# Optimization experiments

Measured on AMD Instinct MI355X. Metric: run time of the kernel, lower is better.

Reference implementation:

```python
import jax, jax.numpy as jnp
import numpy as np

B = 32; LS = 512; LABEL = 256; PRED = 256; LD = 512   # LD = LS//2 + PRED
CIN = 21; COUT = 21; D = 512; H = 8; E = 64; M = 64   # M = top frequency modes
DFF = 2048; LE = 2; MARK = 4; K = 25; EPS = 1e-5


def moving_mean(x):
    # series_decomp moving average: edge-replicate pad then window mean (via cumsum)
    p = (K - 1) // 2
    xp = jnp.pad(x, ((0, 0), (p, p), (0, 0)), mode='edge')
    c = jnp.cumsum(xp, axis=1)
    c = jnp.concatenate([jnp.zeros_like(c[:, :1]), c], axis=1)
    return (c[:, K:] - c[:, :-K]) / K


def decomp(x):
    m = moving_mean(x)
    return x - m, m   # (high/seasonal, low/trend)


def circ_conv(x, k):  # x [B,L,C], k [3,C,O], kernel-3 circular conv, no bias
    xp = jnp.pad(x, ((0, 0), (1, 1), (0, 0)), mode='wrap')
    return jax.lax.conv_general_dilated(xp, k, (1,), 'VALID', dimension_numbers=('NWC', 'WIO', 'NWC'))


def embed(x, mark, ck, tw):  # DataEmbedding_wo_pos: token conv + timeF linear
    return circ_conv(x, ck) + mark @ tw


def heads(x):  # [B,L,D] -> [B,L,H,E]
    return x.reshape(x.shape[0], x.shape[1], H, E)


def freq_self(q, wre, wim):  # FrequencyAdaptiveAttention; q [B,L,H,E]
    L = q.shape[1]
    x = jnp.transpose(q, (0, 2, 3, 1))            # [B,H,E,L]
    xf = jnp.fft.rfft(x, axis=-1)                 # [B,H,E,Lf]
    amp = jnp.mean(jnp.abs(xf), axis=(0, 1, 2))   # adaptive mode selection
    _, idx = jax.lax.top_k(amp, M)
    xs = xf[..., idx]                             # [B,H,E,M]
    w = (wre + 1j * wim).astype(xs.dtype)         # [H,E,E,M] complex
    outs = jnp.einsum('bhem,heom->bhom', xs, w)
    oft = jnp.zeros(xf.shape, xf.dtype).at[..., idx].set(outs)
    y = jnp.fft.irfft(oft, n=L, axis=-1)
    return jnp.transpose(y, (0, 3, 1, 2))         # [B,L,H,E]


def freq_cross(q, k, wre, wim):  # AlignmentFrequencyAttention
    Lq = q.shape[1]
    qf = jnp.fft.rfft(jnp.transpose(q, (0, 2, 3, 1)), axis=-1)
    kf = jnp.fft.rfft(jnp.transpose(k, (0, 2, 3, 1)), axis=-1)
    _, qi = jax.lax.top_k(jnp.mean(jnp.abs(qf), axis=(0, 1, 2)), M)
    _, ki = jax.lax.top_k(jnp.mean(jnp.abs(kf), axis=(0, 1, 2)), M)
    qs = qf[..., qi]; ks = kf[..., ki]            # [B,H,E,M]
    qk = jnp.tanh(jnp.einsum('bhex,bhey->bhxy', qs, ks))
    qkv = jnp.einsum('bhxy,bhey->bhex', qk, ks)
    w = (wre + 1j * wim).astype(qs.dtype)
    outs = jnp.einsum('bhex,heox->bhox', qkv, w)
    oft = jnp.zeros(qf.shape, qf.dtype).at[..., qi].set(outs)
    y = jnp.fft.irfft(oft / (D * D), n=Lq, axis=-1)
    return jnp.transpose(y, (0, 3, 1, 2))


def my_layernorm(x, g, b):  # LN then subtract time-mean (Autoformer my_Layernorm)
    mu = jnp.mean(x, -1, keepdims=True)
    var = jnp.var(x, -1, keepdims=True)
    xh = (x - mu) * jax.lax.rsqrt(var + EPS) * g + b
    return xh - jnp.mean(xh, axis=1, keepdims=True)


def _forward(x_enc, x_mark_enc, x_dec, x_mark_dec, emb_enc_k, emb_enc_t, emb_dec_k, emb_dec_t, fw_enc_re, fw_enc_im, fw_dec_re, fw_dec_im, fw_cr_re, fw_cr_im, enc_Wq, enc_bq, enc_Wo, enc_bo, enc_c1, enc_c2, enc_ng, enc_nb, ds_Wq, ds_bq, ds_Wo, ds_bo, dc_Wq, dc_bq, dc_Wk, dc_bk, dc_Wo, dc_bo, dec_c1, dec_c2, dec_tp, dec_ng, dec_nb, proj_W, proj_b):
    mean = jnp.broadcast_to(jnp.mean(x_enc, axis=1, keepdims=True), (B, PRED, CIN))
    high_init, low_init = decomp(x_enc)
    low_init = jnp.concatenate([low_init[:, -LABEL:, :], mean], axis=1)       # [B,LD,CIN]
    high_init = jnp.pad(high_init[:, -LABEL:, :], ((0, 0), (0, PRED), (0, 0)))
    # encoder
    enc = embed(x_enc, x_mark_enc, emb_enc_k, emb_enc_t)                      # [B,LS,D]
    for i in range(LE):
        a = freq_self(heads(enc @ enc_Wq[i] + enc_bq[i]), fw_enc_re, fw_enc_im)
        a = a.reshape(B, LS, D) @ enc_Wo[i] + enc_bo[i]
        x1, _ = decomp(enc + a)
        y = jax.nn.gelu(x1 @ enc_c1[i]) @ enc_c2[i]
        enc, _ = decomp(x1 + y)
    enc = my_layernorm(enc, enc_ng, enc_nb)
    # decoder (1 layer)
    dec = embed(high_init, x_mark_dec, emb_dec_k, emb_dec_t)                  # [B,LD,D]
    a = freq_self(heads(dec @ ds_Wq + ds_bq), fw_dec_re, fw_dec_im)
    a = a.reshape(B, LD, D) @ ds_Wo + ds_bo
    x1, t1 = decomp(dec + a)
    c = freq_cross(heads(x1 @ dc_Wq + dc_bq), heads(enc @ dc_Wk + dc_bk), fw_cr_re, fw_cr_im)
    c = c.reshape(B, LD, D) @ dc_Wo + dc_bo
    x2, t2 = decomp(x1 + c)
    y = jax.nn.gelu(x2 @ dec_c1) @ dec_c2
    x3, t3 = decomp(x2 + y)
    low_part = low_init + circ_conv(t1 + t2 + t3, dec_tp)                     # trend branch
    high_part = my_layernorm(x3, dec_ng, dec_nb) @ proj_W + proj_b            # seasonal branch
    return (low_part + high_part)[:, -PRED:, :]


def setup_inputs():
    key = jax.random.key(0)
    ks = jax.random.split(key, 32)
    r = lambda i, shape, s=1.0: jax.random.normal(ks[i], shape, dtype=jnp.float32) * s
    z = lambda shape: jnp.zeros(shape, jnp.float32)
    sd = D ** -0.5
    return {
        'x_enc': r(0, (B, LS, CIN)), 'x_mark_enc': r(1, (B, LS, MARK)),
        'x_dec': r(2, (B, LD, CIN)), 'x_mark_dec': r(3, (B, LD, MARK)),
        'emb_enc_k': r(4, (3, CIN, D), 0.1), 'emb_enc_t': r(5, (MARK, D), 0.1),
        'emb_dec_k': r(6, (3, CIN, D), 0.1), 'emb_dec_t': r(7, (MARK, D), 0.1),
        'fw_enc_re': r(8, (H, E, E, M), 0.02), 'fw_enc_im': r(9, (H, E, E, M), 0.02),
        'fw_dec_re': r(10, (H, E, E, M), 0.02), 'fw_dec_im': r(11, (H, E, E, M), 0.02),
        'fw_cr_re': r(12, (H, E, E, M), 0.02), 'fw_cr_im': r(13, (H, E, E, M), 0.02),
        'enc_Wq': r(14, (LE, D, D), sd), 'enc_bq': z((LE, D)),
        'enc_Wo': r(15, (LE, D, D), sd), 'enc_bo': z((LE, D)),
        'enc_c1': r(16, (LE, D, DFF), sd), 'enc_c2': r(17, (LE, DFF, D), DFF ** -0.5),
        'enc_ng': jnp.ones((D,), jnp.float32), 'enc_nb': z((D,)),
        'ds_Wq': r(18, (D, D), sd), 'ds_bq': z((D,)),
        'ds_Wo': r(19, (D, D), sd), 'ds_bo': z((D,)),
        'dc_Wq': r(20, (D, D), sd), 'dc_bq': z((D,)),
        'dc_Wk': r(21, (D, D), sd), 'dc_bk': z((D,)),
        'dc_Wo': r(22, (D, D), sd), 'dc_bo': z((D,)),
        'dec_c1': r(23, (D, DFF), sd), 'dec_c2': r(24, (DFF, D), DFF ** -0.5),
        'dec_tp': r(25, (3, D, COUT), sd),
        'dec_ng': jnp.ones((D,), jnp.float32), 'dec_nb': z((D,)),
        'proj_W': r(26, (D, COUT), sd), 'proj_b': z((COUT,)),
    }


def reference(x_enc, x_mark_enc, x_dec, x_mark_dec, emb_enc_k, emb_enc_t, emb_dec_k, emb_dec_t, fw_enc_re, fw_enc_im, fw_dec_re, fw_dec_im, fw_cr_re, fw_cr_im, enc_Wq, enc_bq, enc_Wo, enc_bo, enc_c1, enc_c2, enc_ng, enc_nb, ds_Wq, ds_bq, ds_Wo, ds_bo, dc_Wq, dc_bq, dc_Wk, dc_bk, dc_Wo, dc_bo, dec_c1, dec_c2, dec_tp, dec_ng, dec_nb, proj_W, proj_b):
    return _forward(x_enc, x_mark_enc, x_dec, x_mark_dec, emb_enc_k, emb_enc_t, emb_dec_k, emb_dec_t, fw_enc_re, fw_enc_im, fw_dec_re, fw_dec_im, fw_cr_re, fw_cr_im, enc_Wq, enc_bq, enc_Wo, enc_bo, enc_c1, enc_c2, enc_ng, enc_nb, ds_Wq, ds_bq, ds_Wo, ds_bo, dc_Wq, dc_bq, dc_Wk, dc_bk, dc_Wo, dc_bo, dec_c1, dec_c2, dec_tp, dec_ng, dec_nb, proj_W, proj_b)
```

## Files before the change

kernel.cpp:

```cpp
#include <hip/hip_runtime.h>
#include <math.h>

#define B_    32
#define LQ    512
#define CIN_  21
#define COUT_ 21
#define D_    512
#define H_    8
#define E_    64
#define M_    64
#define DFF_  2048
#define MARK_ 4
#define KWIN  25
#define PW    12
#define LF    257
#define PRED_ 256
#define EPS_  1e-5f

static __device__ __forceinline__ int iclamp(int v, int lo, int hi) {
  return v < lo ? lo : (v > hi ? hi : v);
}

__global__ void k_dft_tables(float* __restrict__ cosF, float* __restrict__ negsinF,
                             float* __restrict__ c512, float* __restrict__ s512) {
  int i = blockIdx.x * 256 + threadIdx.x;
  if (i < 512) {
    float th = (float)i * (6.283185307179586f / 512.0f);
    c512[i] = cosf(th);
    s512[i] = sinf(th);
  }
  if (i >= 512 * LF) return;
  int t = i / LF, f = i % LF;
  int r = (t * f) & 511;
  float th = (float)r * (6.283185307179586f / 512.0f);
  cosF[i] = cosf(th);
  negsinF[i] = -sinf(th);
}

__global__ void k_enc_decomp(const float* __restrict__ x,
                             float* __restrict__ lowi, float* __restrict__ highi) {
  int b = blockIdx.x, c = threadIdx.x;
  if (c >= CIN_) return;
  const float* xb = x + (long)b * LQ * CIN_ + c;
  float s = 0.f;
  for (int t = 0; t < LQ; t++) s += xb[(long)t * CIN_];
  float mean = s / (float)LQ;
  for (int t = 256; t < LQ; t++) {
    float w = 0.f;
    for (int j = t - PW; j <= t + PW; j++) {
      int jj = iclamp(j, 0, LQ - 1);
      w += xb[(long)jj * CIN_];
    }
    float m = w * (1.f / KWIN);
    lowi [((long)b * LQ + (t - 256)) * CIN_ + c] = m;
    highi[((long)b * LQ + (t - 256)) * CIN_ + c] = xb[(long)t * CIN_] - m;
  }
  for (int t = 256; t < LQ; t++) {
    lowi [((long)b * LQ + t) * CIN_ + c] = mean;
    highi[((long)b * LQ + t) * CIN_ + c] = 0.f;
  }
}

__global__ void k_embed(const float* __restrict__ x, const float* __restrict__ mark,
                        const float* __restrict__ ck, const float* __restrict__ tw,
                        float* __restrict__ out) {
  int o = blockIdx.x * 256 + threadIdx.x;
  int t = blockIdx.y, b = blockIdx.z;
  float acc = 0.f;
  const float* xb = x + (long)b * LQ * CIN_;
  #pragma unroll
  for (int j = 0; j < 3; j++) {
    int tt = (t + j - 1 + LQ) & (LQ - 1);
    const float* xr = xb + (long)tt * CIN_;
    const float* kr = ck + (long)(j * CIN_) * D_ + o;
    for (int c = 0; c < CIN_; c++) acc = fmaf(xr[c], kr[(long)c * D_], acc);
  }
  const float* mr = mark + ((long)b * LQ + t) * MARK_;
  #pragma unroll
  for (int mm = 0; mm < MARK_; mm++) acc = fmaf(mr[mm], tw[(long)mm * D_ + o], acc);
  out[((long)b * LQ + t) * D_ + o] = acc;
}

template<int ACT>
__global__ __launch_bounds__(256) void k_gemm(
    const float* __restrict__ A, const float* __restrict__ Bm,
    const float* __restrict__ bias, float* __restrict__ C,
    int Mr, int Nd, int Kd) {
  constexpr int BM = 128, BN = 128, BK = 32, SA = BM + 1;
  __shared__ float As[BK][SA];
  __shared__ float Bs[BK][BN];
  int m0 = blockIdx.y * BM, n0 = blockIdx.x * BN;
  int tid = threadIdx.x;
  int tx = tid & 15, ty = tid >> 4;
  float acc[8][8] = {};
  const float* Ag = A + (long)m0 * Kd;
  for (int k0 = 0; k0 < Kd; k0 += BK) {
    #pragma unroll
    for (int r = 0; r < 4; r++) {
      int slot = tid + r * 256;
      int row = slot >> 3, k4 = slot & 7;
      const float4 v = *(const float4*)&Ag[(long)row * Kd + k0 + k4 * 4];
      As[k4 * 4 + 0][row] = v.x; As[k4 * 4 + 1][row] = v.y;
      As[k4 * 4 + 2][row] = v.z; As[k4 * 4 + 3][row] = v.w;
    }
    #pragma unroll
    for (int r = 0; r < 4; r++) {
      int slot = tid + r * 256;
      int kk = slot >> 5, n4 = slot & 31;
      *(float4*)&Bs[kk][n4 * 4] = *(const float4*)&Bm[(long)(k0 + kk) * Nd + n0 + n4 * 4];
    }
    __syncthreads();
    #pragma unroll
    for (int kk = 0; kk < BK; kk++) {
      float av[8], bv[8];
      #pragma unroll
      for (int i = 0; i < 8; i++) av[i] = As[kk][ty * 8 + i];
      #pragma unroll
      for (int j = 0; j < 8; j++) bv[j] = Bs[kk][tx * 8 + j];
      #pragma unroll
      for (int i = 0; i < 8; i++)
        #pragma unroll
        for (int j = 0; j < 8; j++)
          acc[i][j] = fmaf(av[i], bv[j], acc[i][j]);
    }
    __syncthreads();
  }
  float bj[8];
  #pragma unroll
  for (int j = 0; j < 8; j++) bj[j] = bias ? bias[n0 + tx * 8 + j] : 0.f;
  #pragma unroll
  for (int i = 0; i < 8; i++) {
    long gm = m0 + ty * 8 + i;
    float* Crow = C + gm * Nd + n0 + tx * 8;
    #pragma unroll
    for (int j4 = 0; j4 < 2; j4++) {
      float4 v;
      float t0[4];
      #pragma unroll
      for (int j = 0; j < 4; j++) {
        float x = acc[i][j4 * 4 + j] + bj[j4 * 4 + j];
        if (ACT == 1) {
          float x3 = x * x * x;
          float th = tanhf(0.7978845608028654f * (x + 0.044715f * x3));
          x = 0.5f * x * (1.f + th);
        }
        t0[j] = x;
      }
      v.x = t0[0]; v.y = t0[1]; v.z = t0[2]; v.w = t0[3];
      *(float4*)&Crow[j4 * 4] = v;
    }
  }
}

__global__ void k_zero(float* __restrict__ p, int n) {
  int i = blockIdx.x * 256 + threadIdx.x;
  if (i < n) p[i] = 0.f;
}

__global__ __launch_bounds__(256) void k_specamp(
    const float* __restrict__ X, const float* __restrict__ cosT,
    const float* __restrict__ nsinT, float* __restrict__ amp) {
  int m0 = blockIdx.y * 64, n0 = blockIdx.x * 64;
  int tid = threadIdx.x, tx = tid & 15, ty = tid >> 4;
  __shared__ float As[32][64];
  __shared__ float Cs[32][65];
  __shared__ float Ss[32][65];
  float aR[4][4] = {}, aI[4][4] = {};
  int b = m0 >> 9, d0 = m0 & 511;
  const float* Xb = X + (long)b * LQ * D_ + d0;
  for (int k0 = 0; k0 < 512; k0 += 32) {
    {
      int mm = tid & 63, kk0 = tid >> 6;
      #pragma unroll
      for (int r = 0; r < 8; r++) {
        int kk = kk0 + r * 4;
        As[kk][mm] = Xb[(long)(k0 + kk) * D_ + mm];
      }
    }
    {
      int nn = tid & 63, kk0 = tid >> 6;
      #pragma unroll
      for (int r = 0; r < 8; r++) {
        int kk = kk0 + r * 4;
        int gn = n0 + nn;
        float c = 0.f, s = 0.f;
        if (gn < LF) { long a = (long)(k0 + kk) * LF + gn; c = cosT[a]; s = nsinT[a]; }
        Cs[kk][nn] = c; Ss[kk][nn] = s;
      }
    }
    __syncthreads();
    #pragma unroll
    for (int kk = 0; kk < 32; kk++) {
      float av[4], cv[4], sv[4];
      #pragma unroll
      for (int i = 0; i < 4; i++) av[i] = As[kk][ty * 4 + i];
      #pragma unroll
      for (int j = 0; j < 4; j++) { cv[j] = Cs[kk][tx * 4 + j]; sv[j] = Ss[kk][tx * 4 + j]; }
      #pragma unroll
      for (int i = 0; i < 4; i++)
        #pragma unroll
        for (int j = 0; j < 4; j++) {
          aR[i][j] = fmaf(av[i], cv[j], aR[i][j]);
          aI[i][j] = fmaf(av[i], sv[j], aI[i][j]);
        }
    }
    __syncthreads();
  }
  __shared__ float csum[64];
  if (tid < 64) csum[tid] = 0.f;
  __syncthreads();
  #pragma unroll
  for (int j = 0; j < 4; j++) {
    float s = 0.f;
    #pragma unroll
    for (int i = 0; i < 4; i++) s += sqrtf(aR[i][j] * aR[i][j] + aI[i][j] * aI[i][j]);
    atomicAdd(&csum[tx * 4 + j], s);
  }
  __syncthreads();
  if (tid < 64 && n0 + tid < LF) atomicAdd(&amp[n0 + tid], csum[tid]);
}

__global__ void k_topk(const float* __restrict__ amp, int* __restrict__ idx) {
  __shared__ float v[512];
  __shared__ float rv[512];
  __shared__ int   ri[512];
  int tid = threadIdx.x;
  v[tid] = (tid < LF) ? amp[tid] : -INFINITY;
  __syncthreads();
  for (int k = 0; k < M_; k++) {
    rv[tid] = v[tid]; ri[tid] = tid;
    __syncthreads();
    for (int st = 256; st > 0; st >>= 1) {
      if (tid < st) {
        float a = rv[tid], b = rv[tid + st];
        int ai = ri[tid], bi = ri[tid + st];
        if (b > a || (b == a && bi < ai)) { rv[tid] = b; ri[tid] = bi; }
      }
      __syncthreads();
    }
    if (tid == 0) { idx[k] = ri[0]; v[ri[0]] = -INFINITY; }
    __syncthreads();
  }
}

__global__ __launch_bounds__(256) void k_gatherdft(
    const float* __restrict__ X, const float* __restrict__ cosT,
    const float* __restrict__ nsinT, const int* __restrict__ idx,
    float* __restrict__ gR, float* __restrict__ gI) {
  int m0 = blockIdx.x * 64;
  int tid = threadIdx.x, tx = tid & 15, ty = tid >> 4;
  __shared__ float As[32][64];
  __shared__ float Cs[32][65];
  __shared__ float Ss[32][65];
  __shared__ int fsel[64];
  if (tid < 64) fsel[tid] = idx[tid];
  __syncthreads();
  float aR[4][4] = {}, aI[4][4] = {};
  int b = m0 >> 9, d0 = m0 & 511;
  const float* Xb = X + (long)b * LQ * D_ + d0;
  for (int k0 = 0; k0 < 512; k0 += 32) {
    {
      int mm = tid & 63, kk0 = tid >> 6;
      #pragma unroll
      for (int r = 0; r < 8; r++) {
        int kk = kk0 + r * 4;
        As[kk][mm] = Xb[(long)(k0 + kk) * D_ + mm];
      }
    }
    {
      int nn = tid & 63, kk0 = tid >> 6;
      int f = fsel[nn];
      #pragma unroll
      for (int r = 0; r < 8; r++) {
        int kk = kk0 + r * 4;
        long a = (long)(k0 + kk) * LF + f;
        Cs[kk][nn] = cosT[a]; Ss[kk][nn] = nsinT[a];
      }
    }
    __syncthreads();
    #pragma unroll
    for (int kk = 0; kk < 32; kk++) {
      float av[4], cv[4], sv[4];
      #pragma unroll
      for (int i = 0; i < 4; i++) av[i] = As[kk][ty * 4 + i];
      #pragma unroll
      for (int j = 0; j < 4; j++) { cv[j] = Cs[kk][tx * 4 + j]; sv[j] = Ss[kk][tx * 4 + j]; }
      #pragma unroll
      for (int i = 0; i < 4; i++)
        #pragma unroll
        for (int j = 0; j < 4; j++) {
          aR[i][j] = fmaf(av[i], cv[j], aR[i][j]);
          aI[i][j] = fmaf(av[i], sv[j], aI[i][j]);
        }
    }
    __syncthreads();
  }
  #pragma unroll
  for (int i = 0; i < 4; i++) {
    long row = m0 + ty * 4 + i;
    #pragma unroll
    for (int j = 0; j < 4; j++) {
      gR[row * 64 + tx * 4 + j] = aR[i][j];
      gI[row * 64 + tx * 4 + j] = aI[i][j];
    }
  }
}

__global__ __launch_bounds__(256) void k_modemix(
    const float* __restrict__ sre, const float* __restrict__ sim,
    const float* __restrict__ wre, const float* __restrict__ wim,
    float* __restrict__ ore, float* __restrict__ oim) {
  int b = blockIdx.z, h = blockIdx.y, oc = blockIdx.x;
  int m = threadIdx.x, osub = threadIdx.y;
  int o = oc * 4 + osub;
  __shared__ float xr[E_][M_], xi[E_][M_];
  #pragma unroll
  for (int r = 0; r < 16; r++) {
    int e = r * 4 + osub;
    long a = ((long)(b * H_ + h) * E_ + e) * M_ + m;
    xr[e][m] = sre[a]; xi[e][m] = sim[a];
  }
  __syncthreads();
  float ar = 0.f, ai = 0.f;
  const float* wrb = wre + ((long)(h * E_) * E_ + o) * M_ + m;
  const float* wib = wim + ((long)(h * E_) * E_ + o) * M_ + m;
  #pragma unroll 4
  for (int e = 0; e < E_; e++) {
    float wr = wrb[(long)e * E_ * M_], wi = wib[(long)e * E_ * M_];
    float qr = xr[e][m], qi = xi[e][m];
    ar = fmaf(qr, wr, ar); ar = fmaf(-qi, wi, ar);
    ai = fmaf(qr, wi, ai); ai = fmaf(qi, wr, ai);
  }
  long oaddr = ((long)(b * H_ + h) * E_ + o) * M_ + m;
  ore[oaddr] = ar; oim[oaddr] = ai;
}

__global__ __launch_bounds__(512) void k_irfft(
    const float* __restrict__ ore, const float* __restrict__ oim,
    const int* __restrict__ idx, const float* __restrict__ c512,
    const float* __restrict__ s512, float scale, float* __restrict__ out) {
  int d = blockIdx.x, b = blockIdx.y, t = threadIdx.x;
  int h = d >> 6, o = d & 63;
  __shared__ float mr[M_], mi[M_];
  __shared__ int   mf[M_];
  __shared__ float cs[512], sn[512];
  cs[t] = c512[t]; sn[t] = s512[t];
  if (t < M_) {
    long a = ((long)(b * H_ + h) * E_ + o) * M_ + t;
    int f = idx[t];
    mf[t] = f;
    float c = (f == 0 || f == 256) ? 1.f : 2.f;
    mr[t] = ore[a] * c; mi[t] = oim[a] * c;
  }
  __syncthreads();
  float acc = 0.f;
  #pragma unroll 8
  for (int m = 0; m < M_; m++) {
    int r = (mf[m] * t) & 511;
    acc += mr[m] * cs[r] - mi[m] * sn[r];
  }
  out[((long)b * LQ + t) * D_ + d] = acc * scale;
}

__global__ void k_decomp(const float* __restrict__ a, const float* __restrict__ bsrc,
                         float* __restrict__ season, float* __restrict__ trend,
                         int trendMode) {
  int c = blockIdx.x * 256 + threadIdx.x;
  int t = blockIdx.y, b = blockIdx.z;
  long base = (long)b * LQ * D_ + c;
  float s = 0.f;
  #pragma unroll
  for (int j = -PW; j <= PW; j++) {
    int tt = iclamp(t + j, 0, LQ - 1);
    float v = a[base + (long)tt * D_];
    if (bsrc) v += bsrc[base + (long)tt * D_];
    s += v;
  }
  float m = s * (1.f / KWIN);
  float cur = a[base + (long)t * D_];
  if (bsrc) cur += bsrc[base + (long)t * D_];
  season[base + (long)t * D_] = cur - m;
  if (trendMode == 1) trend[base + (long)t * D_] = m;
  else if (trendMode == 2) trend[base + (long)t * D_] += m;
}

__global__ __launch_bounds__(256) void k_ln(const float* __restrict__ x,
                                            const float* __restrict__ g,
                                            const float* __restrict__ bt,
                                            float* __restrict__ out) {
  long row = blockIdx.x;
  const float* xr = x + row * D_;
  float v1 = xr[threadIdx.x], v2 = xr[threadIdx.x + 256];
  __shared__ float rs[256], rq[256];
  rs[threadIdx.x] = v1 + v2;
  rq[threadIdx.x] = v1 * v1 + v2 * v2;
  __syncthreads();
  for (int st = 128; st > 0; st >>= 1) {
    if (threadIdx.x < st) { rs[threadIdx.x] += rs[threadIdx.x + st]; rq[threadIdx.x] += rq[threadIdx.x + st]; }
    __syncthreads();
  }
  float mu = rs[0] / (float)D_;
  float var = fmaxf(rq[0] / (float)D_ - mu * mu, 0.f);
  float inv = rsqrtf(var + EPS_);
  out[row * D_ + threadIdx.x]       = (v1 - mu) * inv * g[threadIdx.x]       + bt[threadIdx.x];
  out[row * D_ + threadIdx.x + 256] = (v2 - mu) * inv * g[threadIdx.x + 256] + bt[threadIdx.x + 256];
}

__global__ void k_tmsub(const float* __restrict__ x, float* __restrict__ out) {
  int dcol = blockIdx.x * 256 + threadIdx.x, b = blockIdx.y;
  long base = (long)b * LQ * D_ + dcol;
  float s = 0.f;
  for (int t = 0; t < LQ; t++) s += x[base + (long)t * D_];
  float mu = s / (float)LQ;
  for (int t = 0; t < LQ; t++) out[base + (long)t * D_] = x[base + (long)t * D_] - mu;
}

__global__ __launch_bounds__(256) void k_qk(
    const float* __restrict__ qR, const float* __restrict__ qI,
    const float* __restrict__ kR, const float* __restrict__ kI,
    float* __restrict__ qkre, float* __restrict__ qkim) {
  int b = blockIdx.z, h = blockIdx.y, xc = blockIdx.x;
  int y = threadIdx.x, xs4 = threadIdx.y;
  __shared__ float ksr[E_][64], ksi[E_][64];
  __shared__ float qsr[E_][16], qsi[E_][16];
  long base = (long)(b * H_ + h) * E_;
  int tid = threadIdx.y * 64 + threadIdx.x;
  #pragma unroll
  for (int r = 0; r < 16; r++) {
    int e = r * 4 + xs4;
    long a = (base + e) * 64 + y;
    ksr[e][y] = kR[a]; ksi[e][y] = kI[a];
  }
  #pragma unroll
  for (int r = 0; r < 4; r++) {
    int ii = tid + r * 256;
    int e = ii >> 4, xl = ii & 15;
    long a = (base + e) * 64 + xc * 16 + xl;
    qsr[e][xl] = qR[a]; qsi[e][xl] = qI[a];
  }
  __syncthreads();
  #pragma unroll
  for (int xi = 0; xi < 4; xi++) {
    int xl = xs4 * 4 + xi;
    float ar = 0.f, ai = 0.f;
    for (int e = 0; e < E_; e++) {
      float a1 = qsr[e][xl], b1 = qsi[e][xl], c1 = ksr[e][y], d1 = ksi[e][y];
      ar += a1 * c1 - b1 * d1;
      ai += a1 * d1 + b1 * c1;
    }
    float s = tanhf(ar), t = tanf(ai);
    float t2 = t * t;
    float den = 1.f + s * s * t2;
    float outr = s * (1.f + t2) / den;
    float outi = t * (1.f - s * s) / den;
    int x = xc * 16 + xl;
    long oa = ((long)(b * H_ + h) * M_ + y) * M_ + x;
    qkre[oa] = outr; qkim[oa] = outi;
  }
}

__global__ __launch_bounds__(256) void k_qkv(
    const float* __restrict__ qkre, const float* __restrict__ qkim,
    const float* __restrict__ kR, const float* __restrict__ kI,
    float* __restrict__ vre, float* __restrict__ vim) {
  int b = blockIdx.z, h = blockIdx.y, ec = blockIdx.x;
  int x = threadIdx.x, es = threadIdx.y;
  int e = ec * 4 + es;
  __shared__ float qr[M_][M_], qi2[M_][M_];
  int tid = threadIdx.y * 64 + threadIdx.x;
  #pragma unroll
  for (int r = 0; r < 16; r++) {
    int ii = tid + r * 256;
    int yy = ii >> 6, xx = ii & 63;
    long a = ((long)(b * H_ + h) * M_ + yy) * M_ + xx;
    qr[yy][xx] = qkre[a]; qi2[yy][xx] = qkim[a];
  }
  __syncthreads();
  float ar = 0.f, ai = 0.f;
  long kbase = ((long)(b * H_ + h) * E_ + e) * 64;
  for (int y = 0; y < M_; y++) {
    float c1 = kR[kbase + y], d1 = kI[kbase + y];
    float a1 = qr[y][x], b1 = qi2[y][x];
    ar += a1 * c1 - b1 * d1;
    ai += a1 * d1 + b1 * c1;
  }
  long o = ((long)(b * H_ + h) * E_ + e) * M_ + x;
  vre[o] = ar; vim[o] = ai;
}

__global__ __launch_bounds__(256) void k_final(
    const float* __restrict__ lowi, const float* __restrict__ tsum,
    const float* __restrict__ tp, const float* __restrict__ ln3,
    const float* __restrict__ projW, const float* __restrict__ projb,
    float* __restrict__ out) {
  int o = threadIdx.x;
  int rowi = blockIdx.x * 8 + threadIdx.y;
  int b = rowi >> 8, tpi = rowi & 255;
  int t = tpi + 256;
  if (o >= COUT_) return;
  float acc = lowi[((long)b * LQ + t) * CIN_ + o] + projb[o];
  #pragma unroll
  for (int j = 0; j < 3; j++) {
    int tt = (t + j - 1 + LQ) & (LQ - 1);
    const float* xr = tsum + ((long)b * LQ + tt) * D_;
    const float* kr = tp + (long)(j * D_) * COUT_ + o;
    for (int c = 0; c < D_; c++) acc = fmaf(xr[c], kr[(long)c * COUT_], acc);
  }
  const float* lr = ln3 + ((long)b * LQ + t) * D_;
  for (int d0 = 0; d0 < D_; d0++) acc = fmaf(lr[d0], projW[(long)d0 * COUT_ + o], acc);
  out[((long)b * PRED_ + tpi) * COUT_ + o] = acc;
}

extern "C" void kernel_launch(void* const* d_in, const int* in_sizes, int n_in,
                              void* d_out, int out_size, void* d_ws, size_t ws_size,
                              hipStream_t stream) {
  const float* x_enc      = (const float*)d_in[0];
  const float* x_mark_enc = (const float*)d_in[1];
  const float* x_mark_dec = (const float*)d_in[3];
  const float* emb_enc_k  = (const float*)d_in[4];
  const float* emb_enc_t  = (const float*)d_in[5];
  const float* emb_dec_k  = (const float*)d_in[6];
  const float* emb_dec_t  = (const float*)d_in[7];
  const float* fw_enc_re  = (const float*)d_in[8];
  const float* fw_enc_im  = (const float*)d_in[9];
  const float* fw_dec_re  = (const float*)d_in[10];
  const float* fw_dec_im  = (const float*)d_in[11];
  const float* fw_cr_re   = (const float*)d_in[12];
  const float* fw_cr_im   = (const float*)d_in[13];
  const float* enc_Wq     = (const float*)d_in[14];
  const float* enc_bq     = (const float*)d_in[15];
  const float* enc_Wo     = (const float*)d_in[16];
  const float* enc_bo     = (const float*)d_in[17];
  const float* enc_c1     = (const float*)d_in[18];
  const float* enc_c2     = (const float*)d_in[19];
  const float* enc_ng     = (const float*)d_in[20];
  const float* enc_nb     = (const float*)d_in[21];
  const float* ds_Wq      = (const float*)d_in[22];
  const float* ds_bq      = (const float*)d_in[23];
  const float* ds_Wo      = (const float*)d_in[24];
  const float* ds_bo      = (const float*)d_in[25];
  const float* dc_Wq      = (const float*)d_in[26];
  const float* dc_bq      = (const float*)d_in[27];
  const float* dc_Wk      = (const float*)d_in[28];
  const float* dc_bk      = (const float*)d_in[29];
  const float* dc_Wo      = (const float*)d_in[30];
  const float* dc_bo      = (const float*)d_in[31];
  const float* dec_c1     = (const float*)d_in[32];
  const float* dec_c2     = (const float*)d_in[33];
  const float* dec_tp     = (const float*)d_in[34];
  const float* dec_ng     = (const float*)d_in[35];
  const float* dec_nb     = (const float*)d_in[36];
  const float* proj_W     = (const float*)d_in[37];
  const float* proj_b     = (const float*)d_in[38];
  float* out = (float*)d_out;
  float* ws  = (float*)d_ws;

  constexpr size_t BIG = (size_t)B_ * LQ * D_;
  constexpr size_t OUS = (size_t)B_ * H_ * E_ * M_;
  size_t o = 0;
  auto nxt = [&](size_t n) { size_t r = o; o += (n + 255) & ~(size_t)255; return r; };
  size_t oA = nxt(BIG), oB = nxt(BIG), oC = nxt(BIG), oTS = nxt(BIG);
  size_t oQSR = nxt(OUS), oQSI = nxt(OUS), oKSR = nxt(OUS), oKSI = nxt(OUS),
         oOR = nxt(OUS), oOI = nxt(OUS), oQKR = nxt(OUS), oQKI = nxt(OUS);
  size_t oCOS = nxt((size_t)512 * LF), oNSN = nxt((size_t)512 * LF);
  size_t oC5 = nxt(512), oS5 = nxt(512);
  size_t oAMP = nxt(512), oIQ = nxt(64), oIK = nxt(64);
  size_t oLOW = nxt((size_t)B_ * LQ * CIN_), oHI = nxt((size_t)B_ * LQ * CIN_);
  size_t oFF = nxt(0);
  int FCH = 2048;
  if ((oFF + (size_t)16384 * DFF_) * 4 <= ws_size)      FCH = 16384;
  else if ((oFF + (size_t)4096 * DFF_) * 4 <= ws_size)  FCH = 4096;
  (void)in_sizes; (void)n_in; (void)out_size;

  int* idxq = (int*)(ws + oIQ);
  int* idxk = (int*)(ws + oIK);

  auto GEMM = [&](const float* Ap, const float* Bp, const float* bias,
                  float* Cp, int Mr, int Nd, int Kd, int act) {
    dim3 g(Nd / 128, Mr / 128, 1);
    if (act) k_gemm<1><<<g, dim3(256), 0, stream>>>(Ap, Bp, bias, Cp, Mr, Nd, Kd);
    else     k_gemm<0><<<g, dim3(256), 0, stream>>>(Ap, Bp, bias, Cp, Mr, Nd, Kd);
  };
  auto AMPSEL = [&](const float* x, int* idxp) {
    k_zero<<<2, 256, 0, stream>>>(ws + oAMP, 512);
    k_specamp<<<dim3(5, 256), 256, 0, stream>>>(x, ws + oCOS, ws + oNSN, ws + oAMP);
    k_topk<<<1, 512, 0, stream>>>(ws + oAMP, idxp);
  };
  auto GATHER = [&](const float* x, const int* idxp, float* gR, float* gI) {
    k_gatherdft<<<256, 256, 0, stream>>>(x, ws + oCOS, ws + oNSN, idxp, gR, gI);
  };
  auto MODEMIX = [&](const float* sR, const float* sI, const float* wre, const float* wim) {
    k_modemix<<<dim3(16, H_, B_), dim3(64, 4), 0, stream>>>(sR, sI, wre, wim, ws + oOR, ws + oOI);
  };
  auto IRFFT = [&](const int* idxp, float scale, float* dst) {
    k_irfft<<<dim3(D_, B_), 512, 0, stream>>>(ws + oOR, ws + oOI, idxp,
                                              ws + oC5, ws + oS5, scale, dst);
  };
  auto DECOMP = [&](const float* a, const float* bsrc, float* season, float* trend, int mode) {
    k_decomp<<<dim3(2, LQ, B_), 256, 0, stream>>>(a, bsrc, season, trend, mode);
  };
  auto FFNP = [&](const float* x, const float* c1, const float* c2, float* y) {
    for (int ch = 0; ch < (B_ * LQ) / FCH; ch++) {
      GEMM(x + (size_t)ch * FCH * D_, c1, nullptr, ws + oFF, FCH, DFF_, D_, 1);
      GEMM(ws + oFF, c2, nullptr, y + (size_t)ch * FCH * D_, FCH, D_, DFF_, 0);
    }
  };

  k_dft_tables<<<(512 * LF + 255) / 256, 256, 0, stream>>>(ws + oCOS, ws + oNSN,
                                                           ws + oC5, ws + oS5);
  k_enc_decomp<<<B_, 32, 0, stream>>>(x_enc, ws + oLOW, ws + oHI);
  k_embed<<<dim3(2, LQ, B_), 256, 0, stream>>>(x_enc, x_mark_enc, emb_enc_k, emb_enc_t, ws + oA);

  for (int i = 0; i < 2; i++) {
    GEMM(ws + oA, enc_Wq + (size_t)i * D_ * D_, enc_bq + (size_t)i * D_, ws + oB, B_ * LQ, D_, D_, 0);
    AMPSEL(ws + oB, idxq);
    GATHER(ws + oB, idxq, ws + oQSR, ws + oQSI);
    MODEMIX(ws + oQSR, ws + oQSI, fw_enc_re, fw_enc_im);
    IRFFT(idxq, 1.f / 512.f, ws + oB);
    GEMM(ws + oB, enc_Wo + (size_t)i * D_ * D_, enc_bo + (size_t)i * D_, ws + oC, B_ * LQ, D_, D_, 0);
    DECOMP(ws + oA, ws + oC, ws + oB, nullptr, 0);
    FFNP(ws + oB, enc_c1 + (size_t)i * D_ * DFF_, enc_c2 + (size_t)i * DFF_ * D_, ws + oC);
    DECOMP(ws + oB, ws + oC, ws + oA, nullptr, 0);
  }
  k_ln<<<B_ * LQ, 256, 0, stream>>>(ws + oA, enc_ng, enc_nb, ws + oB);
  k_tmsub<<<dim3(2, B_), 256, 0, stream>>>(ws + oB, ws + oA);

  GEMM(ws + oA, dc_Wk, dc_bk, ws + oB, B_ * LQ, D_, D_, 0);
  AMPSEL(ws + oB, idxk);
  GATHER(ws + oB, idxk, ws + oKSR, ws + oKSI);

  k_embed<<<dim3(2, LQ, B_), 256, 0, stream>>>(ws + oHI, x_mark_dec, emb_dec_k, emb_dec_t, ws + oA);
  GEMM(ws + oA, ds_Wq, ds_bq, ws + oB, B_ * LQ, D_, D_, 0);
  AMPSEL(ws + oB, idxq);
  GATHER(ws + oB, idxq, ws + oQSR, ws + oQSI);
  MODEMIX(ws + oQSR, ws + oQSI, fw_dec_re, fw_dec_im);
  IRFFT(idxq, 1.f / 512.f, ws + oB);
  GEMM(ws + oB, ds_Wo, ds_bo, ws + oC, B_ * LQ, D_, D_, 0);
  DECOMP(ws + oA, ws + oC, ws + oB, ws + oTS, 1);

  GEMM(ws + oB, dc_Wq, dc_bq, ws + oC, B_ * LQ, D_, D_, 0);
  AMPSEL(ws + oC, idxq);
  GATHER(ws + oC, idxq, ws + oQSR, ws + oQSI);
  k_qk<<<dim3(4, H_, B_), dim3(64, 4), 0, stream>>>(
      ws + oQSR, ws + oQSI, ws + oKSR, ws + oKSI, ws + oQKR, ws + oQKI);
  k_qkv<<<dim3(16, H_, B_), dim3(64, 4), 0, stream>>>(
      ws + oQKR, ws + oQKI, ws + oKSR, ws + oKSI, ws + oQSR, ws + oQSI);
  MODEMIX(ws + oQSR, ws + oQSI, fw_cr_re, fw_cr_im);
  IRFFT(idxq, 1.f / (512.f * 262144.f), ws + oC);
  GEMM(ws + oC, dc_Wo, dc_bo, ws + oA, B_ * LQ, D_, D_, 0);
  DECOMP(ws + oB, ws + oA, ws + oC, ws + oTS, 2);
  FFNP(ws + oC, dec_c1, dec_c2, ws + oA);
  DECOMP(ws + oC, ws + oA, ws + oB, ws + oTS, 2);
  k_ln<<<B_ * LQ, 256, 0, stream>>>(ws + oB, dec_ng, dec_nb, ws + oA);
  k_tmsub<<<dim3(2, B_), 256, 0, stream>>>(ws + oA, ws + oC);
  k_final<<<dim3(B_ * PRED_ / 8), dim3(32, 8), 0, stream>>>(
      ws + oLOW, ws + oTS, dec_tp, ws + oC, proj_W, proj_b, out);
}
```

Before: 10.04 ms.

## Store full DFT spectrum during amplitude pass and gather top modes from it

The amplitude kernel now writes the full real/imag spectrum (plus a separate Nyquist column) into scratch buffers. The selected modes are then gathered from that spectrum instead of recomputing a second DFT GEMM. The DFT table is padded to width 320 so tiles can use float4 loads, and the tile size grows to 128x64 with a shared-memory reduction in place of shared atomics. The decomposition kernel switches to a sliding-window running sum over 64 timesteps per thread. In exchange it adds large scratch writes and reads and reuses activation buffers as scratch.

```diff
diff --git a/kernel.cpp b/kernel.cpp
--- a/kernel.cpp
+++ b/kernel.cpp
@@ -14,8 +14,10 @@
 #define KWIN  25
 #define PW    12
 #define LF    257
+#define TW    320
 #define PRED_ 256
 #define EPS_  1e-5f
+#define SPECH (16384 * 256)
 
 static __device__ __forceinline__ int iclamp(int v, int lo, int hi) {
   return v < lo ? lo : (v > hi ? hi : v);
@@ -29,8 +31,9 @@
     c512[i] = cosf(th);
     s512[i] = sinf(th);
   }
-  if (i >= 512 * LF) return;
-  int t = i / LF, f = i % LF;
+  if (i >= 512 * TW) return;
+  int t = i / TW, f = i % TW;
+  if (f >= LF) { cosF[i] = 0.f; negsinF[i] = 0.f; return; }
   int r = (t * f) & 511;
   float th = (float)r * (6.283185307179586f / 512.0f);
   cosF[i] = cosf(th);
@@ -157,47 +160,45 @@
   if (i < n) p[i] = 0.f;
 }
 
-__global__ __launch_bounds__(256) void k_specamp(
-    const float* __restrict__ X, const float* __restrict__ cosT,
-    const float* __restrict__ nsinT, float* __restrict__ amp) {
-  int m0 = blockIdx.y * 64, n0 = blockIdx.x * 64;
+__global__ __launch_bounds__(256) void k_dftamp(
+    const float* __restrict__ X, const float* __restrict__ cosP,
+    const float* __restrict__ nsinP, float* __restrict__ specR,
+    float* __restrict__ specI, float* __restrict__ nyqR,
+    float* __restrict__ nyqI, float* __restrict__ amp) {
+  constexpr int BK = 32;
+  __shared__ float As[BK][132];
+  __shared__ float Cs[BK][68];
+  __shared__ float Ss[BK][68];
+  int m0 = blockIdx.x * 128;
+  int n0 = blockIdx.y * 64;
   int tid = threadIdx.x, tx = tid & 15, ty = tid >> 4;
-  __shared__ float As[32][64];
-  __shared__ float Cs[32][65];
-  __shared__ float Ss[32][65];
-  float aR[4][4] = {}, aI[4][4] = {};
   int b = m0 >> 9, d0 = m0 & 511;
   const float* Xb = X + (long)b * LQ * D_ + d0;
-  for (int k0 = 0; k0 < 512; k0 += 32) {
-    {
-      int mm = tid & 63, kk0 = tid >> 6;
+  float aR[8][4] = {}, aI[8][4] = {};
+  for (int k0 = 0; k0 < 512; k0 += BK) {
+    #pragma unroll
+    for (int r = 0; r < 4; r++) {
+      int slot = tid + r * 256;
+      int kk = slot >> 5, d4 = slot & 31;
+      *(float4*)&As[kk][d4 * 4] = *(const float4*)&Xb[(long)(k0 + kk) * D_ + d4 * 4];
+    }
+    #pragma unroll
+    for (int r = 0; r < 2; r++) {
+      int slot = tid + r * 256;
+      int kk = slot >> 4, f4 = slot & 15;
+      *(float4*)&Cs[kk][f4 * 4] = *(const float4*)&cosP [(long)(k0 + kk) * TW + n0 + f4 * 4];
+      *(float4*)&Ss[kk][f4 * 4] = *(const float4*)&nsinP[(long)(k0 + kk) * TW + n0 + f4 * 4];
+    }
+    __syncthreads();
+    #pragma unroll
+    for (int kk = 0; kk < BK; kk++) {
+      float av[8], cv[4], sv[4];
+      *(float4*)&av[0] = *(const float4*)&As[kk][ty * 8];
+      *(float4*)&av[4] = *(const float4*)&As[kk][ty * 8 + 4];
+      *(float4*)&cv[0] = *(const float4*)&Cs[kk][tx * 4];
+      *(float4*)&sv[0] = *(const float4*)&Ss[kk][tx * 4];
       #pragma unroll
-      for (int r = 0; r < 8; r++) {
-        int kk = kk0 + r * 4;
-        As[kk][mm] = Xb[(long)(k0 + kk) * D_ + mm];
-      }
-    }
-    {
-      int nn = tid & 63, kk0 = tid >> 6;
-      #pragma unroll
-      for (int r = 0; r < 8; r++) {
-        int kk = kk0 + r * 4;
-        int gn = n0 + nn;
-        float c = 0.f, s = 0.f;
-        if (gn < LF) { long a = (long)(k0 + kk) * LF + gn; c = cosT[a]; s = nsinT[a]; }
-        Cs[kk][nn] = c; Ss[kk][nn] = s;
-      }
-    }
-    __syncthreads();
-    #pragma unroll
-    for (int kk = 0; kk < 32; kk++) {
-      float av[4], cv[4], sv[4];
-      #pragma unroll
-      for (int i = 0; i < 4; i++) av[i] = As[kk][ty * 4 + i];
-      #pragma unroll
-      for (int j = 0; j < 4; j++) { cv[j] = Cs[kk][tx * 4 + j]; sv[j] = Ss[kk][tx * 4 + j]; }
-      #pragma unroll
-      for (int i = 0; i < 4; i++)
+      for (int i = 0; i < 8; i++)
         #pragma unroll
         for (int j = 0; j < 4; j++) {
           aR[i][j] = fmaf(av[i], cv[j], aR[i][j]);
@@ -206,18 +207,34 @@
     }
     __syncthreads();
   }
-  __shared__ float csum[64];
-  if (tid < 64) csum[tid] = 0.f;
-  __syncthreads();
+  int c0 = n0 + tx * 4;
+  #pragma unroll
+  for (int i = 0; i < 8; i++) {
+    long row = m0 + ty * 8 + i;
+    if (c0 < 256) {
+      *(float4*)&specR[row * 256 + c0] = make_float4(aR[i][0], aR[i][1], aR[i][2], aR[i][3]);
+      *(float4*)&specI[row * 256 + c0] = make_float4(aI[i][0], aI[i][1], aI[i][2], aI[i][3]);
+    } else if (c0 == 256) {
+      nyqR[row] = aR[i][0];
+      nyqI[row] = aI[i][0];
+    }
+  }
+  __shared__ float csum[16][68];
   #pragma unroll
   for (int j = 0; j < 4; j++) {
     float s = 0.f;
     #pragma unroll
-    for (int i = 0; i < 4; i++) s += sqrtf(aR[i][j] * aR[i][j] + aI[i][j] * aI[i][j]);
-    atomicAdd(&csum[tx * 4 + j], s);
+    for (int i = 0; i < 8; i++)
+      s += sqrtf(aR[i][j] * aR[i][j] + aI[i][j] * aI[i][j]);
+    csum[ty][tx * 4 + j] = s;
   }
   __syncthreads();
-  if (tid < 64 && n0 + tid < LF) atomicAdd(&amp[n0 + tid], csum[tid]);
+  if (tid < 64) {
+    float s = 0.f;
+    #pragma unroll
+    for (int r = 0; r < 16; r++) s += csum[r][tid];
+    if (n0 + tid < LF) atomicAdd(&amp[n0 + tid], s);
+  }
 }
 
 __global__ void k_topk(const float* __restrict__ amp, int* __restrict__ idx) {
@@ -243,67 +260,17 @@
   }
 }
 
-__global__ __launch_bounds__(256) void k_gatherdft(
-    const float* __restrict__ X, const float* __restrict__ cosT,
-    const float* __restrict__ nsinT, const int* __restrict__ idx,
-    float* __restrict__ gR, float* __restrict__ gI) {
-  int m0 = blockIdx.x * 64;
-  int tid = threadIdx.x, tx = tid & 15, ty = tid >> 4;
-  __shared__ float As[32][64];
-  __shared__ float Cs[32][65];
-  __shared__ float Ss[32][65];
-  __shared__ int fsel[64];
-  if (tid < 64) fsel[tid] = idx[tid];
-  __syncthreads();
-  float aR[4][4] = {}, aI[4][4] = {};
-  int b = m0 >> 9, d0 = m0 & 511;
-  const float* Xb = X + (long)b * LQ * D_ + d0;
-  for (int k0 = 0; k0 < 512; k0 += 32) {
-    {
-      int mm = tid & 63, kk0 = tid >> 6;
-      #pragma unroll
-      for (int r = 0; r < 8; r++) {
-        int kk = kk0 + r * 4;
-        As[kk][mm] = Xb[(long)(k0 + kk) * D_ + mm];
-      }
-    }
-    {
-      int nn = tid & 63, kk0 = tid >> 6;
-      int f = fsel[nn];
-      #pragma unroll
-      for (int r = 0; r < 8; r++) {
-        int kk = kk0 + r * 4;
-        long a = (long)(k0 + kk) * LF + f;
-        Cs[kk][nn] = cosT[a]; Ss[kk][nn] = nsinT[a];
-      }
-    }
-    __syncthreads();
-    #pragma unroll
-    for (int kk = 0; kk < 32; kk++) {
-      float av[4], cv[4], sv[4];
-      #pragma unroll
-      for (int i = 0; i < 4; i++) av[i] = As[kk][ty * 4 + i];
-      #pragma unroll
-      for (int j = 0; j < 4; j++) { cv[j] = Cs[kk][tx * 4 + j]; sv[j] = Ss[kk][tx * 4 + j]; }
-      #pragma unroll
-      for (int i = 0; i < 4; i++)
-        #pragma unroll
-        for (int j = 0; j < 4; j++) {
-          aR[i][j] = fmaf(av[i], cv[j], aR[i][j]);
-          aI[i][j] = fmaf(av[i], sv[j], aI[i][j]);
-        }
-    }
-    __syncthreads();
-  }
-  #pragma unroll
-  for (int i = 0; i < 4; i++) {
-    long row = m0 + ty * 4 + i;
-    #pragma unroll
-    for (int j = 0; j < 4; j++) {
-      gR[row * 64 + tx * 4 + j] = aR[i][j];
-      gI[row * 64 + tx * 4 + j] = aI[i][j];
-    }
-  }
+__global__ void k_gathercols(const float* __restrict__ specR, const float* __restrict__ specI,
+                             const float* __restrict__ nyqR, const float* __restrict__ nyqI,
+                             const int* __restrict__ idx,
+                             float* __restrict__ gR, float* __restrict__ gI) {
+  int tid = threadIdx.x;
+  int m = tid & 63, r = tid >> 6;
+  long row = (long)blockIdx.x * 4 + r;
+  int f = idx[m];
+  long o = row * 64 + m;
+  if (f < 256) { gR[o] = specR[row * 256 + f]; gI[o] = specI[row * 256 + f]; }
+  else         { gR[o] = nyqR[row];            gI[o] = nyqI[row]; }
 }
 
 __global__ __launch_bounds__(256) void k_modemix(
@@ -366,22 +333,28 @@
                          float* __restrict__ season, float* __restrict__ trend,
                          int trendMode) {
   int c = blockIdx.x * 256 + threadIdx.x;
-  int t = blockIdx.y, b = blockIdx.z;
+  int t0 = blockIdx.y * 64;
+  int b = blockIdx.z;
   long base = (long)b * LQ * D_ + c;
   float s = 0.f;
-  #pragma unroll
-  for (int j = -PW; j <= PW; j++) {
-    int tt = iclamp(t + j, 0, LQ - 1);
+  for (int j = t0 - PW; j <= t0 + PW; j++) {
+    int tt = iclamp(j, 0, LQ - 1);
     float v = a[base + (long)tt * D_];
     if (bsrc) v += bsrc[base + (long)tt * D_];
     s += v;
   }
-  float m = s * (1.f / KWIN);
-  float cur = a[base + (long)t * D_];
-  if (bsrc) cur += bsrc[base + (long)t * D_];
-  season[base + (long)t * D_] = cur - m;
-  if (trendMode == 1) trend[base + (long)t * D_] = m;
-  else if (trendMode == 2) trend[base + (long)t * D_] += m;
+  for (int t = t0; t < t0 + 64; t++) {
+    float cur = a[base + (long)t * D_];
+    if (bsrc) cur += bsrc[base + (long)t * D_];
+    float m = s * (1.f / KWIN);
+    season[base + (long)t * D_] = cur - m;
+    if (trendMode == 1) trend[base + (long)t * D_] = m;
+    else if (trendMode == 2) trend[base + (long)t * D_] += m;
+    int tn = iclamp(t + PW + 1, 0, LQ - 1), to = iclamp(t - PW, 0, LQ - 1);
+    float vn = a[base + (long)tn * D_], vo = a[base + (long)to * D_];
+    if (bsrc) { vn += bsrc[base + (long)tn * D_]; vo += bsrc[base + (long)to * D_]; }
+    s += vn - vo;
+  }
 }
 
 __global__ __launch_bounds__(256) void k_ln(const float* __restrict__ x,
@@ -562,9 +535,10 @@
   size_t oA = nxt(BIG), oB = nxt(BIG), oC = nxt(BIG), oTS = nxt(BIG);
   size_t oQSR = nxt(OUS), oQSI = nxt(OUS), oKSR = nxt(OUS), oKSI = nxt(OUS),
          oOR = nxt(OUS), oOI = nxt(OUS), oQKR = nxt(OUS), oQKI = nxt(OUS);
-  size_t oCOS = nxt((size_t)512 * LF), oNSN = nxt((size_t)512 * LF);
+  size_t oCOS = nxt((size_t)512 * TW), oNSN = nxt((size_t)512 * TW);
   size_t oC5 = nxt(512), oS5 = nxt(512);
   size_t oAMP = nxt(512), oIQ = nxt(64), oIK = nxt(64);
+  size_t oNR = nxt(16384), oNI = nxt(16384);
   size_t oLOW = nxt((size_t)B_ * LQ * CIN_), oHI = nxt((size_t)B_ * LQ * CIN_);
   size_t oFF = nxt(0);
   int FCH = 2048;
@@ -581,13 +555,15 @@
     if (act) k_gemm<1><<<g, dim3(256), 0, stream>>>(Ap, Bp, bias, Cp, Mr, Nd, Kd);
     else     k_gemm<0><<<g, dim3(256), 0, stream>>>(Ap, Bp, bias, Cp, Mr, Nd, Kd);
   };
-  auto AMPSEL = [&](const float* x, int* idxp) {
+  auto AMPSEL = [&](const float* x, float* scratch, int* idxp) {
     k_zero<<<2, 256, 0, stream>>>(ws + oAMP, 512);
-    k_specamp<<<dim3(5, 256), 256, 0, stream>>>(x, ws + oCOS, ws + oNSN, ws + oAMP);
+    k_dftamp<<<dim3(128, 5), 256, 0, stream>>>(x, ws + oCOS, ws + oNSN,
+        scratch, scratch + SPECH, ws + oNR, ws + oNI, ws + oAMP);
     k_topk<<<1, 512, 0, stream>>>(ws + oAMP, idxp);
   };
-  auto GATHER = [&](const float* x, const int* idxp, float* gR, float* gI) {
-    k_gatherdft<<<256, 256, 0, stream>>>(x, ws + oCOS, ws + oNSN, idxp, gR, gI);
+  auto GATHER = [&](const float* scratch, const int* idxp, float* gR, float* gI) {
+    k_gathercols<<<4096, 256, 0, stream>>>(scratch, scratch + SPECH,
+        ws + oNR, ws + oNI, idxp, gR, gI);
   };
   auto MODEMIX = [&](const float* sR, const float* sI, const float* wre, const float* wim) {
     k_modemix<<<dim3(16, H_, B_), dim3(64, 4), 0, stream>>>(sR, sI, wre, wim, ws + oOR, ws + oOI);
@@ -597,7 +573,7 @@
                                               ws + oC5, ws + oS5, scale, dst);
   };
   auto DECOMP = [&](const float* a, const float* bsrc, float* season, float* trend, int mode) {
-    k_decomp<<<dim3(2, LQ, B_), 256, 0, stream>>>(a, bsrc, season, trend, mode);
+    k_decomp<<<dim3(D_ / 256, LQ / 64, B_), 256, 0, stream>>>(a, bsrc, season, trend, mode);
   };
   auto FFNP = [&](const float* x, const float* c1, const float* c2, float* y) {
     for (int ch = 0; ch < (B_ * LQ) / FCH; ch++) {
@@ -606,15 +582,15 @@
     }
   };
 
-  k_dft_tables<<<(512 * LF + 255) / 256, 256, 0, stream>>>(ws + oCOS, ws + oNSN,
+  k_dft_tables<<<(512 * TW + 255) / 256, 256, 0, stream>>>(ws + oCOS, ws + oNSN,
                                                            ws + oC5, ws + oS5);
   k_enc_decomp<<<B_, 32, 0, stream>>>(x_enc, ws + oLOW, ws + oHI);
   k_embed<<<dim3(2, LQ, B_), 256, 0, stream>>>(x_enc, x_mark_enc, emb_enc_k, emb_enc_t, ws + oA);
 
   for (int i = 0; i < 2; i++) {
     GEMM(ws + oA, enc_Wq + (size_t)i * D_ * D_, enc_bq + (size_t)i * D_, ws + oB, B_ * LQ, D_, D_, 0);
-    AMPSEL(ws + oB, idxq);
-    GATHER(ws + oB, idxq, ws + oQSR, ws + oQSI);
+    AMPSEL(ws + oB, ws + oC, idxq);
+    GATHER(ws + oC, idxq, ws + oQSR, ws + oQSI);
     MODEMIX(ws + oQSR, ws + oQSI, fw_enc_re, fw_enc_im);
     IRFFT(idxq, 1.f / 512.f, ws + oB);
     GEMM(ws + oB, enc_Wo + (size_t)i * D_ * D_, enc_bo + (size_t)i * D_, ws + oC, B_ * LQ, D_, D_, 0);
@@ -626,21 +602,21 @@
   k_tmsub<<<dim3(2, B_), 256, 0, stream>>>(ws + oB, ws + oA);
 
   GEMM(ws + oA, dc_Wk, dc_bk, ws + oB, B_ * LQ, D_, D_, 0);
-  AMPSEL(ws + oB, idxk);
-  GATHER(ws + oB, idxk, ws + oKSR, ws + oKSI);
+  AMPSEL(ws + oB, ws + oC, idxk);
+  GATHER(ws + oC, idxk, ws + oKSR, ws + oKSI);
 
   k_embed<<<dim3(2, LQ, B_), 256, 0, stream>>>(ws + oHI, x_mark_dec, emb_dec_k, emb_dec_t, ws + oA);
   GEMM(ws + oA, ds_Wq, ds_bq, ws + oB, B_ * LQ, D_, D_, 0);
-  AMPSEL(ws + oB, idxq);
-  GATHER(ws + oB, idxq, ws + oQSR, ws + oQSI);
+  AMPSEL(ws + oB, ws + oC, idxq);
+  GATHER(ws + oC, idxq, ws + oQSR, ws + oQSI);
   MODEMIX(ws + oQSR, ws + oQSI, fw_dec_re, fw_dec_im);
   IRFFT(idxq, 1.f / 512.f, ws + oB);
   GEMM(ws + oB, ds_Wo, ds_bo, ws + oC, B_ * LQ, D_, D_, 0);
   DECOMP(ws + oA, ws + oC, ws + oB, ws + oTS, 1);
 
   GEMM(ws + oB, dc_Wq, dc_bq, ws + oC, B_ * LQ, D_, D_, 0);
-  AMPSEL(ws + oC, idxq);
-  GATHER(ws + oC, idxq, ws + oQSR, ws + oQSI);
+  AMPSEL(ws + oC, ws + oA, idxq);
+  GATHER(ws + oA, idxq, ws + oQSR, ws + oQSI);
   k_qk<<<dim3(4, H_, B_), dim3(64, 4), 0, stream>>>(
       ws + oQSR, ws + oQSI, ws + oKSR, ws + oKSI, ws + oQKR, ws + oQKI);
   k_qkv<<<dim3(16, H_, B_), dim3(64, 4), 0, stream>>>(
```

After: 9.075 ms. 9.6% less time.
